# Optimization experiments

Measured on AMD Instinct MI355X. Metric: run time of the kernel, lower is better.

The kernel has to match this reference:

```python
import jax, jax.numpy as jnp
import numpy as np

C = 64
B, H, W = 2, 128, 512
SCALE = C ** (-0.5)


def conv1x1(x, w, b):
    # x: [B,C,H,W], w: [O,I], b: [O]
    return jnp.einsum('bihw,oi->bohw', x, w) + b[None, :, None, None]


def dwconv3x3(x, w, b):
    # depthwise 3x3, w: [C,1,3,3]
    y = jax.lax.conv_general_dilated(
        x, w, window_strides=(1, 1), padding='SAME',
        feature_group_count=x.shape[1],
        dimension_numbers=('NCHW', 'OIHW', 'NCHW'))
    return y + b[None, :, None, None]


def proj12(x, w1, b1, wd, bd):
    return dwconv3x3(conv1x1(x, w1, b1), wd, bd)


def setup_inputs() -> dict:
    key = jax.random.key(0)
    ks = jax.random.split(key, 32)
    d = {}
    d['x_l'] = jax.random.normal(ks[0], (B, C, H, W), dtype=jnp.float32)
    d['x_r'] = jax.random.normal(ks[1], (B, C, H, W), dtype=jnp.float32)
    i = 2
    for p in ['lp1', 'rp1', 'lp2', 'rp2']:
        d[p + '_w1'] = jax.random.normal(ks[i], (C, C), dtype=jnp.float32) * 0.05; i += 1
        d[p + '_b1'] = jnp.zeros((C,), dtype=jnp.float32)
        d[p + '_wd'] = jax.random.normal(ks[i], (C, 1, 3, 3), dtype=jnp.float32) * 0.1; i += 1
        d[p + '_bd'] = jnp.zeros((C,), dtype=jnp.float32)
    for p in ['lp3', 'rp3']:
        d[p + '_w'] = jax.random.normal(ks[i], (C, C), dtype=jnp.float32) * 0.05; i += 1
        d[p + '_b'] = jnp.zeros((C,), dtype=jnp.float32)
    return d


def reference(x_l, x_r,
              lp1_w1, lp1_b1, lp1_wd, lp1_bd,
              rp1_w1, rp1_b1, rp1_wd, rp1_bd,
              lp2_w1, lp2_b1, lp2_wd, lp2_bd,
              rp2_w1, rp2_b1, rp2_wd, rp2_bd,
              lp3_w, lp3_b, rp3_w, rp3_b):
    Ql = proj12(x_l, lp1_w1, lp1_b1, lp1_wd, lp1_bd)  # [B,C,H,W]
    Qr = proj12(x_r, rp1_w1, rp1_b1, rp1_wd, rp1_bd)  # [B,C,H,W]
    # attention[b,h,w,v] = sum_c Ql[b,c,h,w] * Qr[b,c,h,v]
    att = jnp.einsum('bchw,bchv->bhwv', Ql, Qr) * SCALE  # [B,H,W,W]
    Vl = proj12(x_l, lp2_w1, lp2_b1, lp2_wd, lp2_bd)
    Vr = proj12(x_r, rp2_w1, rp2_b1, rp2_wd, rp2_bd)
    # softmax over right-view width (last axis), aggregate Vr
    A_r2l = jax.nn.softmax(att, axis=-1)
    F_r2l = jnp.einsum('bhwv,bchv->bchw', A_r2l, Vr)  # [B,C,H,W]
    # transposed attention, softmax over left-view width (axis -2 of att)
    A_l2r = jax.nn.softmax(att, axis=-2)
    F_l2r = jnp.einsum('bhwv,bchw->bchv', A_l2r, Vl)  # [B,C,H,W]
    F_r2l = conv1x1(F_r2l, lp3_w, lp3_b)
    F_l2r = conv1x1(F_l2r, rp3_w, rp3_b)
    return x_l + F_r2l + x_r + F_l2r
```

## Files before the change

kernel.cpp:

```cpp
#include <hip/hip_runtime.h>
#include <hip/hip_bf16.h>

typedef __attribute__((ext_vector_type(8))) short short8;
typedef __attribute__((ext_vector_type(4))) float f32x4;

#define QSCALE 0.18033688011112042f

__device__ __forceinline__ unsigned short f2bf(float f){
    unsigned u = __float_as_uint(f);
    unsigned r = (u + 0x7fffu + ((u>>16)&1u))>>16;
    return (unsigned short)r;
}
__device__ __forceinline__ unsigned pk_rtne(float hi, float lo){
    return (((unsigned)f2bf(hi))<<16) | (unsigned)f2bf(lo);
}

__global__ __launch_bounds__(256) void prep_k(const float* __restrict__ xl,
                                              const float* __restrict__ xr,
                                              float* __restrict__ out,
                                              unsigned short* __restrict__ XtL,
                                              unsigned short* __restrict__ XtR){
    __shared__ float ft[64*65];
    int bid = blockIdx.x;
    int strip = bid & 1023, b = bid >> 10;
    int px0 = strip << 6;
    int tid = threadIdx.x;
    float4 vrs[4];
    #pragma unroll
    for (int it=0; it<4; it++){
        int lin = it*256 + tid;
        int c = lin >> 4, piece = lin & 15;
        size_t off = (((size_t)(b*64 + c))<<16) + px0 + piece*4;
        float4 va = *(const float4*)(xl + off);
        float4 vb = *(const float4*)(xr + off);
        vrs[it] = vb;
        float4 vo; vo.x=va.x+vb.x; vo.y=va.y+vb.y; vo.z=va.z+vb.z; vo.w=va.w+vb.w;
        *(float4*)(out + off) = vo;
        float* d = ft + c*65 + piece*4;
        d[0]=va.x; d[1]=va.y; d[2]=va.z; d[3]=va.w;
    }
    __syncthreads();
    #pragma unroll
    for (int it=0; it<2; it++){
        int lin = it*256 + tid;
        int pxl = lin >> 3, cb = lin & 7;
        unsigned r[4];
        #pragma unroll
        for (int j=0;j<4;j++){
            unsigned lo = f2bf(ft[(cb*8 + 2*j  )*65 + pxl]);
            unsigned hi = f2bf(ft[(cb*8 + 2*j+1)*65 + pxl]);
            r[j] = lo | (hi<<16);
        }
        uint4 v; v.x=r[0]; v.y=r[1]; v.z=r[2]; v.w=r[3];
        *(uint4*)(XtL + ((size_t)(b<<16) + px0 + pxl)*64 + cb*8) = v;
    }
    __syncthreads();
    #pragma unroll
    for (int it=0; it<4; it++){
        int lin = it*256 + tid;
        int c = lin >> 4, piece = lin & 15;
        float4 vb = vrs[it];
        float* d = ft + c*65 + piece*4;
        d[0]=vb.x; d[1]=vb.y; d[2]=vb.z; d[3]=vb.w;
    }
    __syncthreads();
    #pragma unroll
    for (int it=0; it<2; it++){
        int lin = it*256 + tid;
        int pxl = lin >> 3, cb = lin & 7;
        unsigned r[4];
        #pragma unroll
        for (int j=0;j<4;j++){
            unsigned lo = f2bf(ft[(cb*8 + 2*j  )*65 + pxl]);
            unsigned hi = f2bf(ft[(cb*8 + 2*j+1)*65 + pxl]);
            r[j] = lo | (hi<<16);
        }
        uint4 v; v.x=r[0]; v.y=r[1]; v.z=r[2]; v.w=r[3];
        *(uint4*)(XtR + ((size_t)(b<<16) + px0 + pxl)*64 + cb*8) = v;
    }
}

__global__ __launch_bounds__(256) void gemm_k(const unsigned short* __restrict__ XtL,
                                              const unsigned short* __restrict__ XtR,
                                              const float* __restrict__ wAL, const float* __restrict__ bAL,
                                              const float* __restrict__ wBL, const float* __restrict__ bBL,
                                              const float* __restrict__ wAR, const float* __restrict__ bAR,
                                              const float* __restrict__ wBR, const float* __restrict__ bBR,
                                              unsigned short* __restrict__ T1L, unsigned short* __restrict__ T2L,
                                              unsigned short* __restrict__ T1R, unsigned short* __restrict__ T2R){
    __shared__ __align__(16) short sB[128*72];
    __shared__ float sbias[128];
    int tid = threadIdx.x;
    int side = blockIdx.x >> 9;
    int px0 = (blockIdx.x & 511) << 8;
    const unsigned short* Xt = side ? XtR : XtL;
    const float* wA = side ? wAR : wAL;  const float* bA = side ? bAR : bAL;
    const float* wB = side ? wBR : wBL;  const float* bB = side ? bBR : bBL;
    unsigned short* T1 = side ? T1R : T1L;
    unsigned short* T2 = side ? T2R : T2L;

    #pragma unroll
    for (int it=0; it<8; it++){
        int lin = it*256 + tid;
        int o = lin >> 4, cc4 = (lin & 15) << 2;
        const float* wsrc = (o < 64) ? (wA + o*64 + cc4) : (wB + (o-64)*64 + cc4);
        float4 w4 = *(const float4*)wsrc;
        uint2 v; v.x = pk_rtne(w4.y, w4.x); v.y = pk_rtne(w4.w, w4.z);
        *(uint2*)(sB + o*72 + cc4) = v;
    }
    if (tid < 128) sbias[tid] = (tid < 64) ? bA[tid] : bB[tid-64];

    int wv = tid>>6, lane = tid&63, quad = lane>>4, l16 = lane&15;
    int m0 = wv*64;
    short8 a0[4], a1[4];
    #pragma unroll
    for (int mt=0; mt<4; mt++){
        size_t row = (size_t)(px0 + m0 + mt*16 + l16)*64;
        a0[mt] = *(const short8*)(Xt + row + quad*8);
        a1[mt] = *(const short8*)(Xt + row + 32 + quad*8);
    }
    __syncthreads();

    const f32x4 z4 = {0.f,0.f,0.f,0.f};
    #pragma unroll
    for (int set=0; set<2; set++){
        unsigned short* T = set ? T2 : T1;
        short8 bB0[4], bB1[4];
        #pragma unroll
        for (int nt=0; nt<4; nt++){
            bB0[nt] = *(const short8*)(sB + (set*64 + nt*16 + l16)*72 + quad*8);
            bB1[nt] = *(const short8*)(sB + (set*64 + nt*16 + l16)*72 + 32 + quad*8);
        }
        f32x4 acc[4][4];
        #pragma unroll
        for (int mt=0; mt<4; mt++)
            #pragma unroll
            for (int nt=0; nt<4; nt++){
                acc[mt][nt] = __builtin_amdgcn_mfma_f32_16x16x32_bf16(a0[mt], bB0[nt], z4, 0,0,0);
                acc[mt][nt] = __builtin_amdgcn_mfma_f32_16x16x32_bf16(a1[mt], bB1[nt], acc[mt][nt], 0,0,0);
            }
        #pragma unroll
        for (int nt=0; nt<4; nt++){
            float bias = sbias[set*64 + nt*16 + l16];
            #pragma unroll
            for (int mt=0; mt<4; mt++){
                #pragma unroll
                for (int r=0;r<4;r++){
                    int pxr = px0 + m0 + mt*16 + quad*4 + r;
                    T[(size_t)pxr*64 + nt*16 + l16] = f2bf(acc[mt][nt][r] + bias);
                }
            }
        }
    }
}

__device__ __forceinline__ void dw_tile(const unsigned short* __restrict__ Tb,
                                        const float* __restrict__ wd,
                                        const float* __restrict__ bd,
                                        int c0, int w0, int h, float acc[4][4]){
    #pragma unroll
    for (int ch=0; ch<4; ch++){
        float bv = bd[c0+ch];
        #pragma unroll
        for (int i=0;i<4;i++) acc[ch][i] = bv;
    }
    #pragma unroll
    for (int dh=-1; dh<=1; dh++){
        int hh = h + dh;
        if (hh < 0 || hh > 127) continue;
        const unsigned short* Tr = Tb + ((size_t)(hh*512))*64 + c0;
        float win[6][4];
        #pragma unroll
        for (int j=0;j<6;j++){
            int ww = w0 - 1 + j;
            if (ww >= 0 && ww < 512){
                uint2 v = *(const uint2*)(Tr + (size_t)ww*64);
                win[j][0] = __uint_as_float(v.x<<16);
                win[j][1] = __uint_as_float(v.x & 0xffff0000u);
                win[j][2] = __uint_as_float(v.y<<16);
                win[j][3] = __uint_as_float(v.y & 0xffff0000u);
            } else {
                win[j][0]=0.f; win[j][1]=0.f; win[j][2]=0.f; win[j][3]=0.f;
            }
        }
        #pragma unroll
        for (int ch=0; ch<4; ch++){
            float k0 = wd[(c0+ch)*9 + (dh+1)*3];
            float k1 = wd[(c0+ch)*9 + (dh+1)*3 + 1];
            float k2 = wd[(c0+ch)*9 + (dh+1)*3 + 2];
            #pragma unroll
            for (int i=0;i<4;i++)
                acc[ch][i] += k0*win[i][ch] + k1*win[i+1][ch] + k2*win[i+2][ch];
        }
    }
}

__global__ __launch_bounds__(256) void dwconv_k(const unsigned short* __restrict__ T1,
                                                const unsigned short* __restrict__ T2,
                                                const float* __restrict__ wd1,
                                                const float* __restrict__ bd1,
                                                const float* __restrict__ wd2,
                                                const float* __restrict__ bd2,
                                                unsigned short* __restrict__ Qdst,
                                                unsigned short* __restrict__ Vdst,
                                                float qscale){
    int bid = blockIdx.x;
    int wt = bid & 7, h = (bid>>3)&127, b = bid>>10;
    int tid = threadIdx.x;
    int cg = tid & 15, wl = tid >> 4;
    int c0 = cg*4;
    int w0 = wt*64 + wl*4;
    float acc[4][4];
    dw_tile(T1 + ((size_t)b<<22), wd1, bd1, c0, w0, h, acc);
    {
        int base = (b*128 + h)*512;
        #pragma unroll
        for (int i=0;i<4;i++){
            uint2 v;
            v.x = pk_rtne(acc[1][i]*qscale, acc[0][i]*qscale);
            v.y = pk_rtne(acc[3][i]*qscale, acc[2][i]*qscale);
            *(uint2*)(Qdst + ((size_t)(base + w0 + i))*64 + c0) = v;
        }
    }
    dw_tile(T2 + ((size_t)b<<22), wd2, bd2, c0, w0, h, acc);
    {
        #pragma unroll
        for (int ch=0; ch<4; ch++){
            uint2 v;
            v.x = pk_rtne(acc[ch][1], acc[ch][0]);
            v.y = pk_rtne(acc[ch][3], acc[ch][2]);
            *(uint2*)(Vdst + (((size_t)(b*64 + c0 + ch))<<16) + h*512 + w0) = v;
        }
    }
}

#define PQ 72
#define PK 72
#define PV 72
#define PP 72
#define PFA 72
#define POT 17
#define OFF_Q   0
#define OFF_K   18432
#define OFF_V   27648
#define LDS_TOT 36864

__global__ __launch_bounds__(256) void flash_k(
    const unsigned short* __restrict__ Ql, const unsigned short* __restrict__ Qr,
    const unsigned short* __restrict__ Vl, const unsigned short* __restrict__ Vr,
    const float* __restrict__ lw3, const float* __restrict__ lb3,
    const float* __restrict__ rw3, const float* __restrict__ rb3,
    float* __restrict__ out)
{
    __shared__ __align__(16) char smem[LDS_TOT];
    short* sK  = (short*)(smem + OFF_K);
    short* sV  = (short*)(smem + OFF_V);
    short* sP  = (short*)(smem + OFF_Q);
    short* sFA = (short*)(smem + OFF_Q);
    float* sOT = (float*)(smem + OFF_K);

    int bid = blockIdx.x;
    int g  = ((bid >> 5) << 3) | (bid & 7);
    int qt = (bid >> 3) & 3;
    int h = g & 127, b = (g >> 7) & 1, dir = g >> 8;
    const unsigned short *Qg, *Kg, *Vg; const float *w3, *b3;
    if (dir==0){ Qg = Ql; Kg = Qr; Vg = Vr; w3 = lw3; b3 = lb3; }
    else       { Qg = Qr; Kg = Ql; Vg = Vl; w3 = rw3; b3 = rb3; }

    int tid = threadIdx.x;
    int wv = tid>>6, lane = tid&63, quad = lane>>4, l16 = lane&15;
    int bh = b*128 + h;

    short8 aq0[2], aq1[2];
    #pragma unroll
    for (int s=0; s<2; s++){
        size_t qrow = ((size_t)bh*512 + qt*128 + wv*32 + s*16 + l16)*64;
        aq0[s] = *(const short8*)(Qg + qrow + quad*8);
        aq1[s] = *(const short8*)(Qg + qrow + 32 + quad*8);
    }

    const f32x4 z4 = {0.f,0.f,0.f,0.f};
    f32x4 oacc[2][4];
    #pragma unroll
    for (int s=0; s<2; s++)
        #pragma unroll
        for (int ct=0; ct<4; ct++) oacc[s][ct] = z4;
    float lps[2] = {0.f, 0.f};

    const uint4* Ksrc = (const uint4*)(Kg + (size_t)bh*512*64);
    const unsigned short* Vbase = Vg + ((size_t)(b*64)*128 + h)*512;

    for (int kt=0; kt<8; kt++){
        #pragma unroll
        for (int it=0; it<2; it++){
            int idx = it*256 + tid;
            int row = idx>>3, piece = idx&7;
            *(uint4*)(sK + row*PK + piece*8) = Ksrc[(size_t)(kt*64 + row)*8 + piece];
            uint4 vv = *(const uint4*)(Vbase + (size_t)row*65536 + kt*64 + piece*8);
            *(uint4*)(sV + row*PV + piece*8) = vv;
        }
        __syncthreads();
        #pragma unroll
        for (int nt=0; nt<4; nt++){
            short8 bk0 = *(const short8*)(sK + (nt*16 + l16)*PK + quad*8);
            short8 bk1 = *(const short8*)(sK + (nt*16 + l16)*PK + 32 + quad*8);
            #pragma unroll
            for (int s=0; s<2; s++){
                __builtin_amdgcn_s_setprio(1);
                f32x4 sv = __builtin_amdgcn_mfma_f32_16x16x32_bf16(bk0, aq0[s], z4, 0,0,0);
                sv       = __builtin_amdgcn_mfma_f32_16x16x32_bf16(bk1, aq1[s], sv, 0,0,0);
                __builtin_amdgcn_s_setprio(0);
                float p0 = __builtin_amdgcn_exp2f(sv[0]);
                float p1 = __builtin_amdgcn_exp2f(sv[1]);
                float p2 = __builtin_amdgcn_exp2f(sv[2]);
                float p3 = __builtin_amdgcn_exp2f(sv[3]);
                lps[s] += (p0+p1) + (p2+p3);
                unsigned lo = __builtin_amdgcn_perm(__float_as_uint(p1), __float_as_uint(p0), 0x07060302);
                unsigned hi = __builtin_amdgcn_perm(__float_as_uint(p3), __float_as_uint(p2), 0x07060302);
                uint2 pv; pv.x = lo; pv.y = hi;
                *(uint2*)(sP + (wv*32 + s*16 + l16)*PP + nt*16 + quad*4) = pv;
            }
        }
        short8 ap0[2], ap1[2];
        #pragma unroll
        for (int s=0; s<2; s++){
            ap0[s] = *(const short8*)(sP + (wv*32 + s*16 + l16)*PP + quad*8);
            ap1[s] = *(const short8*)(sP + (wv*32 + s*16 + l16)*PP + 32 + quad*8);
        }
        __builtin_amdgcn_s_setprio(1);
        #pragma unroll
        for (int ct=0; ct<4; ct++){
            short8 bv0 = *(const short8*)(sV + (ct*16 + l16)*PV + quad*8);
            short8 bv1 = *(const short8*)(sV + (ct*16 + l16)*PV + 32 + quad*8);
            #pragma unroll
            for (int s=0; s<2; s++){
                oacc[s][ct] = __builtin_amdgcn_mfma_f32_16x16x32_bf16(ap0[s], bv0, oacc[s][ct], 0,0,0);
                oacc[s][ct] = __builtin_amdgcn_mfma_f32_16x16x32_bf16(ap1[s], bv1, oacc[s][ct], 0,0,0);
            }
        }
        __builtin_amdgcn_s_setprio(0);
        __syncthreads();
    }

    float inv[2][4];
    #pragma unroll
    for (int s=0; s<2; s++){
        float l = lps[s];
        l += __shfl_xor(l, 16);
        l += __shfl_xor(l, 32);
        #pragma unroll
        for (int r=0;r<4;r++) inv[s][r] = 1.0f / __shfl(l, quad*4 + r);
    }

    #pragma unroll
    for (int s=0; s<2; s++){
        short* sFw = sFA + (wv*32 + s*16)*PFA;
        #pragma unroll
        for (int ct=0; ct<4; ct++){
            #pragma unroll
            for (int r=0;r<4;r++)
                sFw[(quad*4+r)*PFA + ct*16 + l16] = (short)f2bf(oacc[s][ct][r]*inv[s][r]);
        }
    }
    short8 af0[2], af1[2];
    #pragma unroll
    for (int s=0; s<2; s++){
        af0[s] = *(const short8*)(sFA + (wv*32 + s*16 + l16)*PFA + quad*8);
        af1[s] = *(const short8*)(sFA + (wv*32 + s*16 + l16)*PFA + 32 + quad*8);
    }
    f32x4 d2[2][4];
    #pragma unroll
    for (int ot=0; ot<4; ot++){
        const float* wrow = w3 + (ot*16 + l16)*64 + quad*8;
        float4 wa = *(const float4*)(wrow);
        float4 wb = *(const float4*)(wrow + 4);
        float4 wc = *(const float4*)(wrow + 32);
        float4 wd = *(const float4*)(wrow + 36);
        short8 bw0, bw1;
        bw0[0]=(short)f2bf(wa.x); bw0[1]=(short)f2bf(wa.y); bw0[2]=(short)f2bf(wa.z); bw0[3]=(short)f2bf(wa.w);
        bw0[4]=(short)f2bf(wb.x); bw0[5]=(short)f2bf(wb.y); bw0[6]=(short)f2bf(wb.z); bw0[7]=(short)f2bf(wb.w);
        bw1[0]=(short)f2bf(wc.x); bw1[1]=(short)f2bf(wc.y); bw1[2]=(short)f2bf(wc.z); bw1[3]=(short)f2bf(wc.w);
        bw1[4]=(short)f2bf(wd.x); bw1[5]=(short)f2bf(wd.y); bw1[6]=(short)f2bf(wd.z); bw1[7]=(short)f2bf(wd.w);
        float bias = b3[ot*16 + l16];
        #pragma unroll
        for (int s=0; s<2; s++){
            d2[s][ot] = __builtin_amdgcn_mfma_f32_16x16x32_bf16(af0[s], bw0, z4, 0,0,0);
            d2[s][ot] = __builtin_amdgcn_mfma_f32_16x16x32_bf16(af1[s], bw1, d2[s][ot], 0,0,0);
            #pragma unroll
            for (int r=0;r<4;r++) d2[s][ot][r] += bias;
        }
    }
    float* sOw = sOT + wv*(64*POT);
    #pragma unroll
    for (int s=0; s<2; s++){
        #pragma unroll
        for (int ot=0; ot<4; ot++){
            #pragma unroll
            for (int r=0;r<4;r++)
                sOw[(ot*16 + l16)*POT + quad*4 + r] = d2[s][ot][r];
        }
        int qbase = qt*128 + wv*32 + s*16;
        #pragma unroll
        for (int it=0; it<16; it++){
            int o = it*4 + quad;
            float val = sOw[o*POT + l16];
            unsafeAtomicAdd(out + ((size_t)(b*64 + o)*128 + h)*512 + qbase + l16, val);
        }
    }
}

extern "C" void kernel_launch(void* const* d_in, const int* in_sizes, int n_in,
                              void* d_out, int out_size, void* d_ws, size_t ws_size,
                              hipStream_t stream)
{
    const float* xl = (const float*)d_in[0];
    const float* xr = (const float*)d_in[1];
    const float* lp1_w1 = (const float*)d_in[2];
    const float* lp1_b1 = (const float*)d_in[3];
    const float* lp1_wd = (const float*)d_in[4];
    const float* lp1_bd = (const float*)d_in[5];
    const float* rp1_w1 = (const float*)d_in[6];
    const float* rp1_b1 = (const float*)d_in[7];
    const float* rp1_wd = (const float*)d_in[8];
    const float* rp1_bd = (const float*)d_in[9];
    const float* lp2_w1 = (const float*)d_in[10];
    const float* lp2_b1 = (const float*)d_in[11];
    const float* lp2_wd = (const float*)d_in[12];
    const float* lp2_bd = (const float*)d_in[13];
    const float* rp2_w1 = (const float*)d_in[14];
    const float* rp2_b1 = (const float*)d_in[15];
    const float* rp2_wd = (const float*)d_in[16];
    const float* rp2_bd = (const float*)d_in[17];
    const float* lp3_w  = (const float*)d_in[18];
    const float* lp3_b  = (const float*)d_in[19];
    const float* rp3_w  = (const float*)d_in[20];
    const float* rp3_b  = (const float*)d_in[21];
    float* out = (float*)d_out;

    const size_t S = 16777216;
    char* ws = (char*)d_ws;
    unsigned short* s0 = (unsigned short*)(ws);
    unsigned short* s1 = (unsigned short*)(ws + 1*S);
    unsigned short* s2 = (unsigned short*)(ws + 2*S);
    unsigned short* s3 = (unsigned short*)(ws + 3*S);
    unsigned short* s4 = (unsigned short*)(ws + 4*S);
    unsigned short* s5 = (unsigned short*)(ws + 5*S);

    prep_k<<<2048, 256, 0, stream>>>(xl, xr, out, s0, s1);

    gemm_k<<<1024, 256, 0, stream>>>(s0, s1,
        lp1_w1, lp1_b1, lp2_w1, lp2_b1,
        rp1_w1, rp1_b1, rp2_w1, rp2_b1,
        s2, s3, s4, s5);

    dwconv_k<<<2048, 256, 0, stream>>>(s2, s3,
        lp1_wd, lp1_bd, lp2_wd, lp2_bd, s0, s1, QSCALE);

    dwconv_k<<<2048, 256, 0, stream>>>(s4, s5,
        rp1_wd, rp1_bd, rp2_wd, rp2_bd, s2, s3, 1.0f);

    flash_k<<<2048, 256, 0, stream>>>(s0, s2, s1, s3,
        lp3_w, lp3_b, rp3_w, rp3_b, out);
}
```

Before: 324.0 us.

## Fuse input transpose/prep kernel into the 1x1-conv GEMM kernel

Merges the prep kernel (residual sum, transpose and bf16 conversion of both inputs) with the 1x1-conv GEMM kernel. Each block now stages a 64x128 fp32 tile of x_l and then x_r in shared memory and builds MFMA A-operands directly from it, so the bf16 transposed intermediates no longer go through global memory and one launch disappears. The MFMA operand order is also swapped so each lane writes four packed bf16 channels per store instead of scalar stores. The cost is a larger shared-memory footprint per block, strided LDS reads with per-element conversions, and fewer blocks.

New measurement: 309.0 us. 4.6% less time.

```diff
diff --git a/kernel.cpp b/kernel.cpp
--- a/kernel.cpp
+++ b/kernel.cpp
@@ -15,143 +15,124 @@
     return (((unsigned)f2bf(hi))<<16) | (unsigned)f2bf(lo);
 }
 
-__global__ __launch_bounds__(256) void prep_k(const float* __restrict__ xl,
-                                              const float* __restrict__ xr,
-                                              float* __restrict__ out,
-                                              unsigned short* __restrict__ XtL,
-                                              unsigned short* __restrict__ XtR){
-    __shared__ float ft[64*65];
+__global__ __launch_bounds__(256) void prepgemm_k(const float* __restrict__ xl,
+                                                  const float* __restrict__ xr,
+                                                  float* __restrict__ out,
+                                                  const float* __restrict__ wAL, const float* __restrict__ bAL,
+                                                  const float* __restrict__ wBL, const float* __restrict__ bBL,
+                                                  const float* __restrict__ wAR, const float* __restrict__ bAR,
+                                                  const float* __restrict__ wBR, const float* __restrict__ bBR,
+                                                  unsigned short* __restrict__ T1L, unsigned short* __restrict__ T2L,
+                                                  unsigned short* __restrict__ T1R, unsigned short* __restrict__ T2R){
+    __shared__ float ftA[64*130];
+    __shared__ __align__(16) short sB[128*72];
+    __shared__ float sbias[128];
+
     int bid = blockIdx.x;
-    int strip = bid & 1023, b = bid >> 10;
-    int px0 = strip << 6;
+    int b = bid >> 9, px0 = (bid & 511) << 7;
     int tid = threadIdx.x;
-    float4 vrs[4];
-    #pragma unroll
-    for (int it=0; it<4; it++){
+    int wv = tid>>6, lane = tid&63, quad = lane>>4, l16 = lane&15;
+
+    float4 vxr[8];
+    #pragma unroll
+    for (int it=0; it<8; it++){
         int lin = it*256 + tid;
-        int c = lin >> 4, piece = lin & 15;
+        int c = lin >> 5, piece = lin & 31;
         size_t off = (((size_t)(b*64 + c))<<16) + px0 + piece*4;
         float4 va = *(const float4*)(xl + off);
         float4 vb = *(const float4*)(xr + off);
-        vrs[it] = vb;
+        vxr[it] = vb;
         float4 vo; vo.x=va.x+vb.x; vo.y=va.y+vb.y; vo.z=va.z+vb.z; vo.w=va.w+vb.w;
         *(float4*)(out + off) = vo;
-        float* d = ft + c*65 + piece*4;
-        d[0]=va.x; d[1]=va.y; d[2]=va.z; d[3]=va.w;
+        float* d = ftA + c*130 + piece*4;
+        float2 lo; lo.x=va.x; lo.y=va.y;
+        float2 hi; hi.x=va.z; hi.y=va.w;
+        *(float2*)(d) = lo;
+        *(float2*)(d+2) = hi;
+    }
+    {
+        #pragma unroll
+        for (int it=0; it<8; it++){
+            int lin = it*256 + tid;
+            int o = lin >> 4, cc4 = (lin & 15) << 2;
+            const float* wsrc = (o < 64) ? (wAL + o*64 + cc4) : (wBL + (o-64)*64 + cc4);
+            float4 w4 = *(const float4*)wsrc;
+            uint2 v; v.x = pk_rtne(w4.y, w4.x); v.y = pk_rtne(w4.w, w4.z);
+            *(uint2*)(sB + o*72 + cc4) = v;
+        }
+        if (tid < 128) sbias[tid] = (tid < 64) ? bAL[tid] : bBL[tid-64];
     }
     __syncthreads();
-    #pragma unroll
-    for (int it=0; it<2; it++){
-        int lin = it*256 + tid;
-        int pxl = lin >> 3, cb = lin & 7;
-        unsigned r[4];
-        #pragma unroll
-        for (int j=0;j<4;j++){
-            unsigned lo = f2bf(ft[(cb*8 + 2*j  )*65 + pxl]);
-            unsigned hi = f2bf(ft[(cb*8 + 2*j+1)*65 + pxl]);
-            r[j] = lo | (hi<<16);
-        }
-        uint4 v; v.x=r[0]; v.y=r[1]; v.z=r[2]; v.w=r[3];
-        *(uint4*)(XtL + ((size_t)(b<<16) + px0 + pxl)*64 + cb*8) = v;
-    }
+
+    const f32x4 z4 = {0.f,0.f,0.f,0.f};
+
+    #define DO_GEMM(T1p, T2p) do {                                                  \
+        short8 a0[2], a1[2];                                                        \
+        _Pragma("unroll")                                                           \
+        for (int mt=0; mt<2; mt++){                                                 \
+            int pxr = wv*32 + mt*16 + l16;                                          \
+            _Pragma("unroll")                                                       \
+            for (int j=0;j<8;j++){                                                  \
+                a0[mt][j] = (short)f2bf(ftA[(quad*8 + j)*130 + pxr]);               \
+                a1[mt][j] = (short)f2bf(ftA[(32 + quad*8 + j)*130 + pxr]);          \
+            }                                                                       \
+        }                                                                           \
+        _Pragma("unroll")                                                           \
+        for (int set=0; set<2; set++){                                              \
+            unsigned short* T = set ? (T2p) : (T1p);                                \
+            short8 bB0[4], bB1[4];                                                  \
+            _Pragma("unroll")                                                       \
+            for (int nt=0; nt<4; nt++){                                             \
+                bB0[nt] = *(const short8*)(sB + (set*64 + nt*16 + l16)*72 + quad*8);      \
+                bB1[nt] = *(const short8*)(sB + (set*64 + nt*16 + l16)*72 + 32 + quad*8); \
+            }                                                                       \
+            _Pragma("unroll")                                                       \
+            for (int nt=0; nt<4; nt++){                                             \
+                float4 b4 = *(const float4*)(sbias + set*64 + nt*16 + quad*4);      \
+                _Pragma("unroll")                                                   \
+                for (int mt=0; mt<2; mt++){                                         \
+                    f32x4 acc = __builtin_amdgcn_mfma_f32_16x16x32_bf16(bB0[nt], a0[mt], z4, 0,0,0); \
+                    acc       = __builtin_amdgcn_mfma_f32_16x16x32_bf16(bB1[nt], a1[mt], acc, 0,0,0); \
+                    uint2 v;                                                        \
+                    v.x = pk_rtne(acc[1]+b4.y, acc[0]+b4.x);                        \
+                    v.y = pk_rtne(acc[3]+b4.w, acc[2]+b4.z);                        \
+                    int px = px0 + wv*32 + mt*16 + l16;                             \
+                    *(uint2*)(T + (size_t)px*64 + nt*16 + quad*4) = v;              \
+                }                                                                   \
+            }                                                                       \
+        }                                                                           \
+    } while(0)
+
+    DO_GEMM(T1L + ((size_t)b<<22), T2L + ((size_t)b<<22));
     __syncthreads();
-    #pragma unroll
-    for (int it=0; it<4; it++){
-        int lin = it*256 + tid;
-        int c = lin >> 4, piece = lin & 15;
-        float4 vb = vrs[it];
-        float* d = ft + c*65 + piece*4;
-        d[0]=vb.x; d[1]=vb.y; d[2]=vb.z; d[3]=vb.w;
-    }
-    __syncthreads();
-    #pragma unroll
-    for (int it=0; it<2; it++){
-        int lin = it*256 + tid;
-        int pxl = lin >> 3, cb = lin & 7;
-        unsigned r[4];
-        #pragma unroll
-        for (int j=0;j<4;j++){
-            unsigned lo = f2bf(ft[(cb*8 + 2*j  )*65 + pxl]);
-            unsigned hi = f2bf(ft[(cb*8 + 2*j+1)*65 + pxl]);
-            r[j] = lo | (hi<<16);
-        }
-        uint4 v; v.x=r[0]; v.y=r[1]; v.z=r[2]; v.w=r[3];
-        *(uint4*)(XtR + ((size_t)(b<<16) + px0 + pxl)*64 + cb*8) = v;
-    }
-}
-
-__global__ __launch_bounds__(256) void gemm_k(const unsigned short* __restrict__ XtL,
-                                              const unsigned short* __restrict__ XtR,
-                                              const float* __restrict__ wAL, const float* __restrict__ bAL,
-                                              const float* __restrict__ wBL, const float* __restrict__ bBL,
-                                              const float* __restrict__ wAR, const float* __restrict__ bAR,
-                                              const float* __restrict__ wBR, const float* __restrict__ bBR,
-                                              unsigned short* __restrict__ T1L, unsigned short* __restrict__ T2L,
-                                              unsigned short* __restrict__ T1R, unsigned short* __restrict__ T2R){
-    __shared__ __align__(16) short sB[128*72];
-    __shared__ float sbias[128];
-    int tid = threadIdx.x;
-    int side = blockIdx.x >> 9;
-    int px0 = (blockIdx.x & 511) << 8;
-    const unsigned short* Xt = side ? XtR : XtL;
-    const float* wA = side ? wAR : wAL;  const float* bA = side ? bAR : bAL;
-    const float* wB = side ? wBR : wBL;  const float* bB = side ? bBR : bBL;
-    unsigned short* T1 = side ? T1R : T1L;
-    unsigned short* T2 = side ? T2R : T2L;
 
     #pragma unroll
     for (int it=0; it<8; it++){
         int lin = it*256 + tid;
-        int o = lin >> 4, cc4 = (lin & 15) << 2;
-        const float* wsrc = (o < 64) ? (wA + o*64 + cc4) : (wB + (o-64)*64 + cc4);
-        float4 w4 = *(const float4*)wsrc;
-        uint2 v; v.x = pk_rtne(w4.y, w4.x); v.y = pk_rtne(w4.w, w4.z);
-        *(uint2*)(sB + o*72 + cc4) = v;
-    }
-    if (tid < 128) sbias[tid] = (tid < 64) ? bA[tid] : bB[tid-64];
-
-    int wv = tid>>6, lane = tid&63, quad = lane>>4, l16 = lane&15;
-    int m0 = wv*64;
-    short8 a0[4], a1[4];
-    #pragma unroll
-    for (int mt=0; mt<4; mt++){
-        size_t row = (size_t)(px0 + m0 + mt*16 + l16)*64;
-        a0[mt] = *(const short8*)(Xt + row + quad*8);
-        a1[mt] = *(const short8*)(Xt + row + 32 + quad*8);
+        int c = lin >> 5, piece = lin & 31;
+        float4 vb = vxr[it];
+        float* d = ftA + c*130 + piece*4;
+        float2 lo; lo.x=vb.x; lo.y=vb.y;
+        float2 hi; hi.x=vb.z; hi.y=vb.w;
+        *(float2*)(d) = lo;
+        *(float2*)(d+2) = hi;
+    }
+    {
+        #pragma unroll
+        for (int it=0; it<8; it++){
+            int lin = it*256 + tid;
+            int o = lin >> 4, cc4 = (lin & 15) << 2;
+            const float* wsrc = (o < 64) ? (wAR + o*64 + cc4) : (wBR + (o-64)*64 + cc4);
+            float4 w4 = *(const float4*)wsrc;
+            uint2 v; v.x = pk_rtne(w4.y, w4.x); v.y = pk_rtne(w4.w, w4.z);
+            *(uint2*)(sB + o*72 + cc4) = v;
+        }
+        if (tid < 128) sbias[tid] = (tid < 64) ? bAR[tid] : bBR[tid-64];
     }
     __syncthreads();
 
-    const f32x4 z4 = {0.f,0.f,0.f,0.f};
-    #pragma unroll
-    for (int set=0; set<2; set++){
-        unsigned short* T = set ? T2 : T1;
-        short8 bB0[4], bB1[4];
-        #pragma unroll
-        for (int nt=0; nt<4; nt++){
-            bB0[nt] = *(const short8*)(sB + (set*64 + nt*16 + l16)*72 + quad*8);
-            bB1[nt] = *(const short8*)(sB + (set*64 + nt*16 + l16)*72 + 32 + quad*8);
-        }
-        f32x4 acc[4][4];
-        #pragma unroll
-        for (int mt=0; mt<4; mt++)
-            #pragma unroll
-            for (int nt=0; nt<4; nt++){
-                acc[mt][nt] = __builtin_amdgcn_mfma_f32_16x16x32_bf16(a0[mt], bB0[nt], z4, 0,0,0);
-                acc[mt][nt] = __builtin_amdgcn_mfma_f32_16x16x32_bf16(a1[mt], bB1[nt], acc[mt][nt], 0,0,0);
-            }
-        #pragma unroll
-        for (int nt=0; nt<4; nt++){
-            float bias = sbias[set*64 + nt*16 + l16];
-            #pragma unroll
-            for (int mt=0; mt<4; mt++){
-                #pragma unroll
-                for (int r=0;r<4;r++){
-                    int pxr = px0 + m0 + mt*16 + quad*4 + r;
-                    T[(size_t)pxr*64 + nt*16 + l16] = f2bf(acc[mt][nt][r] + bias);
-                }
-            }
-        }
-    }
+    DO_GEMM(T1R + ((size_t)b<<22), T2R + ((size_t)b<<22));
+    #undef DO_GEMM
 }
 
 __device__ __forceinline__ void dw_tile(const unsigned short* __restrict__ Tb,
@@ -446,9 +427,7 @@
     unsigned short* s4 = (unsigned short*)(ws + 4*S);
     unsigned short* s5 = (unsigned short*)(ws + 5*S);
 
-    prep_k<<<2048, 256, 0, stream>>>(xl, xr, out, s0, s1);
-
-    gemm_k<<<1024, 256, 0, stream>>>(s0, s1,
+    prepgemm_k<<<1024, 256, 0, stream>>>(xl, xr, out,
         lp1_w1, lp1_b1, lp2_w1, lp2_b1,
         rp1_w1, rp1_b1, rp2_w1, rp2_b1,
         s2, s3, s4, s5);
```
